# Optimization experiments

Measured on AMD Instinct MI355X. Metric: run time of the kernel, lower is better.

Reference implementation:

```python
import jax, jax.numpy as jnp
import numpy as np

MONOTONICITY = 1.0  # init kwarg monotonicity=1


def _interp_channel(xq, xs, ys):
    """Monotonic piecewise-linear interp for one channel.
    xq: (N,) query points; xs: (B,) sorted breakpoints; ys: (B,) knot values.
    Linear extrapolation beyond both ends using the edge segment slopes.
    """
    B = xs.shape[0]
    # segment index in [1, B-1]; elements below xs[0] / above xs[-1] use edge segments
    idx = jnp.clip(jnp.searchsorted(xs, xq), 1, B - 1)
    x0 = xs[idx - 1]
    x1 = xs[idx]
    y0 = ys[idx - 1]
    y1 = ys[idx]
    slope = (y1 - y0) / (x1 - x0)
    return y0 + slope * (xq - x0)


def setup_inputs() -> dict:
    key = jax.random.key(0)
    k1, k2, k3, k4 = jax.random.split(key, 4)
    N, C, B = 2097152, 16, 32
    x = jax.random.normal(k1, (N, C), dtype=jnp.float32)
    # learned parameters of MonoPointPWL (per channel)
    xp = jax.random.normal(k2, (C, B), dtype=jnp.float32)        # raw x positions (sorted at use)
    y0 = jax.random.normal(k3, (C,), dtype=jnp.float32)          # y value at first knot
    dy = jax.random.normal(k4, (C, B - 1), dtype=jnp.float32)    # raw segment deltas
    return {"x": x, "xp": xp, "y0": y0, "dy": dy}


def reference(x, xp, y0, dy):
    # sorted breakpoint x positions per channel: (C, B)
    xs = jnp.sort(xp, axis=1)
    # monotone knot values: y0 + cumsum(|dy|) * monotonicity, (C, B)
    steps = jnp.abs(dy) * MONOTONICITY
    ys = y0[:, None] + jnp.concatenate(
        [jnp.zeros_like(y0)[:, None], jnp.cumsum(steps, axis=1)], axis=1
    )
    # vectorize over channels: x is (N, C), params are (C, B)
    out = jax.vmap(_interp_channel, in_axes=(1, 0, 0), out_axes=1)(x, xs, ys)
    return out
```

## Files before the change

kernel.cpp:

```cpp
#include <hip/hip_runtime.h>
#include <hip/hip_bf16.h>


#define C_CH 16
#define B_KN 32

#define ROT(k) ((((k) << 2) | ((k) >> 3)) & 31)


__global__ __launch_bounds__(512) void pwl_setup_kernel(
    const float* __restrict__ xp, const float* __restrict__ y0,
    const float* __restrict__ dy, float* __restrict__ ws) {
    __shared__ float s_x[C_CH][B_KN];
    __shared__ float s_xs[C_CH][B_KN];
    __shared__ float s_ys[C_CH][B_KN];
    int t = threadIdx.x;
    int c = t >> 5;
    int k = t & 31;
    float v = xp[c * B_KN + k];
    s_x[c][k] = v;
    __syncthreads();
    int rank = 0;
#pragma unroll
    for (int j = 0; j < B_KN; ++j) {
        float u = s_x[c][j];
        rank += (u < v || (u == v && j < k)) ? 1 : 0;
    }
    s_xs[c][rank] = v;
    float acc = y0[c];
    for (int j = 0; j < k; ++j) acc += fabsf(dy[c * (B_KN - 1) + j]);
    s_ys[c][k] = acc;
    __syncthreads();
    ws[c * B_KN + k] = s_xs[c][k];
    if (k < B_KN - 1) {
        float x0 = s_xs[c][k], x1 = s_xs[c][k + 1];
        float ya = s_ys[c][k], yb = s_ys[c][k + 1];
        float a = (yb - ya) / (x1 - x0);
        float b = ya - a * x0;
        ws[512 + c * B_KN + k]  = a;
        ws[1024 + c * B_KN + k] = b;
    } else {
        ws[512 + c * B_KN + k]  = 0.0f;
        ws[1024 + c * B_KN + k] = 0.0f;
    }
}

__global__ __launch_bounds__(256) void pwl_main_kernel(
    const float4* __restrict__ x, float4* __restrict__ out,
    const float* __restrict__ ws, int n4) {
    __shared__ float s_xs[C_CH][B_KN + 1];
    __shared__ float s_a[C_CH][B_KN + 1];
    __shared__ float s_b[C_CH][B_KN + 1];
    for (int i = threadIdx.x; i < C_CH * B_KN; i += 256) {
        int c = i >> 5, k = i & 31;
        int rk = ROT(k);
        s_xs[c][rk] = ws[i];
        s_a[c][rk]  = ws[512 + i];
        s_b[c][rk]  = ws[1024 + i];
    }
    __syncthreads();

    int tid = blockIdx.x * 256 + threadIdx.x;
    int stride = gridDim.x * 256;
    int c0 = (threadIdx.x & 3) << 2;
    for (int i = tid; i < n4; i += stride) {
        float4 v = x[i];
        float xv[4] = {v.x, v.y, v.z, v.w};
        float r[4];
#pragma unroll
        for (int j = 0; j < 4; ++j) {
            int c = c0 + j;
            float xq = xv[j];
            const float* xs = s_xs[c];
            int pos = 0;
#pragma unroll
            for (int s = 16; s >= 1; s >>= 1) {
                int idx = pos + s - 1;
                pos += (xs[ROT(idx)] < xq) ? s : 0;
            }
            int seg = (pos > 1 ? pos : 1) - 1;
            seg = seg > 30 ? 30 : seg;
            int rseg = ROT(seg);
            r[j] = fmaf(s_a[c][rseg], xq, s_b[c][rseg]);
        }
        out[i] = make_float4(r[0], r[1], r[2], r[3]);
    }
}

extern "C" void kernel_launch(void* const* d_in, const int* in_sizes, int n_in,
                              void* d_out, int out_size, void* d_ws, size_t ws_size,
                              hipStream_t stream) {
    const float* x  = (const float*)d_in[0];
    const float* xp = (const float*)d_in[1];
    const float* y0 = (const float*)d_in[2];
    const float* dy = (const float*)d_in[3];
    float* out = (float*)d_out;
    float* ws  = (float*)d_ws;

    pwl_setup_kernel<<<1, 512, 0, stream>>>(xp, y0, dy, ws);

    int n4 = in_sizes[0] / 4;
    int blocks = (n4 + 255) / 256;
    if (blocks > 2048) blocks = 2048;
    pwl_main_kernel<<<blocks, 256, 0, stream>>>((const float4*)x, (float4*)out, ws, n4);
}
```

Baseline: 52.23 us.

## Fix each thread to one channel and keep binary-search pivots in registers

Each thread now handles scalar elements of a single fixed channel, striding by the grid size, so the top four levels of the per-element binary search use breakpoints held in registers and select chains. Only the last comparison and the coefficient lookup touch LDS, and the slope and intercept are packed into one float2 read. Global accesses change from float4 to scalar float loads and stores, four per iteration. That means more memory instructions for a bandwidth-bound stream, traded against much less LDS traffic.

```diff
diff --git a/kernel.cpp b/kernel.cpp
--- a/kernel.cpp
+++ b/kernel.cpp
@@ -46,44 +46,68 @@
 }
 
 __global__ __launch_bounds__(256) void pwl_main_kernel(
-    const float4* __restrict__ x, float4* __restrict__ out,
-    const float* __restrict__ ws, int n4) {
-    __shared__ float s_xs[C_CH][B_KN + 1];
-    __shared__ float s_a[C_CH][B_KN + 1];
-    __shared__ float s_b[C_CH][B_KN + 1];
-    for (int i = threadIdx.x; i < C_CH * B_KN; i += 256) {
-        int c = i >> 5, k = i & 31;
+    const float* __restrict__ x, float* __restrict__ out,
+    const float* __restrict__ ws, int n) {
+    __shared__ float  s_xs[C_CH][B_KN + 1];
+    __shared__ float2 s_ab[C_CH][B_KN + 1];
+    int t = threadIdx.x;
+    for (int p = t; p < C_CH * B_KN; p += 256) {
+        int c = p >> 5, k = p & 31;
         int rk = ROT(k);
-        s_xs[c][rk] = ws[i];
-        s_a[c][rk]  = ws[512 + i];
-        s_b[c][rk]  = ws[1024 + i];
+        s_xs[c][rk] = ws[p];
+        s_ab[c][rk] = make_float2(ws[512 + p], ws[1024 + p]);
     }
+    int tid = blockIdx.x * 256 + t;
+    int c = tid & 15;
+    const float* xsg = ws + c * B_KN;
+    float v15_ = xsg[15];
+    float v7_  = xsg[7],  v23_ = xsg[23];
+    float v3_  = xsg[3],  v11_ = xsg[11], v19_ = xsg[19], v27_ = xsg[27];
+    float v1_  = xsg[1],  v5_  = xsg[5],  v9_  = xsg[9],  v13_ = xsg[13];
+    float v17_ = xsg[17], v21_ = xsg[21], v25_ = xsg[25], v29_ = xsg[29];
     __syncthreads();
 
-    int tid = blockIdx.x * 256 + threadIdx.x;
-    int stride = gridDim.x * 256;
-    int c0 = (threadIdx.x & 3) << 2;
-    for (int i = tid; i < n4; i += stride) {
-        float4 v = x[i];
-        float xv[4] = {v.x, v.y, v.z, v.w};
-        float r[4];
+    int T = gridDim.x * 256;
+    for (int f = tid; f < n; f += 4 * T) {
+        int f1 = f + T, f2 = f + 2 * T, f3 = f + 3 * T;
+        float x0 = x[f];
+        float x1 = (f1 < n) ? x[f1] : x0;
+        float x2 = (f2 < n) ? x[f2] : x0;
+        float x3 = (f3 < n) ? x[f3] : x0;
+        float xv[4] = {x0, x1, x2, x3};
+        float rr[4];
 #pragma unroll
-        for (int j = 0; j < 4; ++j) {
-            int c = c0 + j;
-            float xq = xv[j];
-            const float* xs = s_xs[c];
-            int pos = 0;
-#pragma unroll
-            for (int s = 16; s >= 1; s >>= 1) {
-                int idx = pos + s - 1;
-                pos += (xs[ROT(idx)] < xq) ? s : 0;
-            }
+        for (int u = 0; u < 4; ++u) {
+            float xq = xv[u];
+            bool b5 = (v15_ < xq);
+            int pos = b5 ? 16 : 0;
+            float t4 = b5 ? v23_ : v7_;
+            bool b4 = (t4 < xq);
+            pos += b4 ? 8 : 0;
+            float ta = b4 ? v11_ : v3_;
+            float tb = b4 ? v27_ : v19_;
+            float t3 = b5 ? tb : ta;
+            bool b3 = (t3 < xq);
+            pos += b3 ? 4 : 0;
+            float u0 = b3 ? v5_  : v1_;
+            float u1 = b3 ? v13_ : v9_;
+            float uu = b4 ? u1 : u0;
+            float w0 = b3 ? v21_ : v17_;
+            float w1 = b3 ? v29_ : v25_;
+            float ww = b4 ? w1 : w0;
+            float z  = b5 ? ww : uu;
+            bool b2 = (z < xq);
+            pos += b2 ? 2 : 0;
+            pos += (s_xs[c][ROT(pos)] < xq) ? 1 : 0;
             int seg = (pos > 1 ? pos : 1) - 1;
             seg = seg > 30 ? 30 : seg;
-            int rseg = ROT(seg);
-            r[j] = fmaf(s_a[c][rseg], xq, s_b[c][rseg]);
+            float2 ab = s_ab[c][ROT(seg)];
+            rr[u] = fmaf(ab.x, xq, ab.y);
         }
-        out[i] = make_float4(r[0], r[1], r[2], r[3]);
+        out[f] = rr[0];
+        if (f1 < n) out[f1] = rr[1];
+        if (f2 < n) out[f2] = rr[2];
+        if (f3 < n) out[f3] = rr[3];
     }
 }
 
@@ -99,8 +123,6 @@
 
     pwl_setup_kernel<<<1, 512, 0, stream>>>(xp, y0, dy, ws);
 
-    int n4 = in_sizes[0] / 4;
-    int blocks = (n4 + 255) / 256;
-    if (blocks > 2048) blocks = 2048;
-    pwl_main_kernel<<<blocks, 256, 0, stream>>>((const float4*)x, (float4*)out, ws, n4);
+    int n = in_sizes[0];
+    pwl_main_kernel<<<2048, 256, 0, stream>>>(x, out, ws, n);
 }
```

Result: slower. 65.86 us (+26.1%).
